# Optimization experiments

Measured on AMD Instinct MI355X. Metric: run time of the kernel, lower is better.

## Reference

```python
import jax, jax.numpy as jnp
import numpy as np

IN_FEATURES = 4096
OUT_FEATURES = 4096


def setup_inputs() -> dict:
    key = jax.random.key(0)
    k1, k2, k3 = jax.random.split(key, 3)
    x = jax.random.normal(k1, (4, 2048, IN_FEATURES), dtype=jnp.float32)
    # int8 quantized weight, stored as int8 (simulating torch int8 Parameter)
    weight_q = jax.random.randint(k2, (OUT_FEATURES, IN_FEATURES), -127, 128, dtype=jnp.int8)
    weight_scaler = jax.random.uniform(k3, (OUT_FEATURES,), dtype=jnp.float32) * 0.02
    return {"x": x, "weight_q": weight_q, "weight_scaler": weight_scaler}


def reference(x, weight_q, weight_scaler):
    # Dequantize: per-output-channel scale broadcast over in_features,
    # then F.linear: out = x @ W^T  (W: [out, in])
    w = weight_q.astype(jnp.float32) * weight_scaler[:, None]  # [out, in]
    return jnp.einsum('bsi,oi->bso', x, w)
```

## Files before the change

kernel.cpp:

```cpp
#include <hip/hip_runtime.h>
#include <stdint.h>
#include <stddef.h>

#define M_DIM 8192
#define N_DIM 4096
#define K_DIM 4096

#define BM 128
#define BN 128
#define BK 128

typedef int i32x4 __attribute__((ext_vector_type(4)));

__device__ __forceinline__ void async_load16(void* lds, const void* g) {
  __builtin_amdgcn_global_load_lds(
      (const __attribute__((address_space(1))) void*)g,
      (__attribute__((address_space(3))) void*)lds,
      16, 0, 0);
}

__global__ void quant_x_kernel(const float* __restrict__ x,
                               signed char* __restrict__ xq,
                               float* __restrict__ xs) {
  const int row = blockIdx.x;
  const float4* xr = (const float4*)(x + (size_t)row * K_DIM);
  const int t = threadIdx.x;
  float4 v[4];
  float m = 0.f;
#pragma unroll
  for (int r = 0; r < 4; ++r) {
    v[r] = xr[r * 256 + t];
    m = fmaxf(m, fmaxf(fmaxf(fabsf(v[r].x), fabsf(v[r].y)),
                       fmaxf(fabsf(v[r].z), fabsf(v[r].w))));
  }
#pragma unroll
  for (int off = 32; off > 0; off >>= 1)
    m = fmaxf(m, __shfl_down(m, off, 64));
  __shared__ float wmax[4];
  if ((t & 63) == 0) wmax[t >> 6] = m;
  __syncthreads();
  float rowmax = fmaxf(fmaxf(wmax[0], wmax[1]), fmaxf(wmax[2], wmax[3]));
  float inv = rowmax > 0.f ? 127.0f / rowmax : 0.f;
  if (t == 0) xs[row] = rowmax > 0.f ? rowmax * (1.0f / 127.0f) : 0.f;
  uint* oq = (uint*)(xq + (size_t)row * K_DIM);
#pragma unroll
  for (int r = 0; r < 4; ++r) {
    union { signed char c[4]; uint u; } o;
    o.c[0] = (signed char)(int)rintf(v[r].x * inv);
    o.c[1] = (signed char)(int)rintf(v[r].y * inv);
    o.c[2] = (signed char)(int)rintf(v[r].z * inv);
    o.c[3] = (signed char)(int)rintf(v[r].w * inv);
    oq[r * 256 + t] = o.u;
  }
}

__global__ void pack_w_kernel(const int* __restrict__ w, signed char* __restrict__ wp) {
  const int4* wi = (const int4*)w;
  uint* wo = (uint*)wp;
  size_t base = (size_t)blockIdx.x * 1024 + threadIdx.x;
#pragma unroll
  for (int r = 0; r < 4; ++r) {
    int4 a = wi[base + r * 256];
    union { signed char c[4]; uint u; } o;
    o.c[0] = (signed char)a.x; o.c[1] = (signed char)a.y;
    o.c[2] = (signed char)a.z; o.c[3] = (signed char)a.w;
    wo[base + r * 256] = o.u;
  }
}

__global__ __launch_bounds__(256, 2) void gemm_i8(
    const signed char* __restrict__ Aq, const signed char* __restrict__ Bq,
    const float* __restrict__ xs, const float* __restrict__ scaler,
    float* __restrict__ C) {
  __shared__ __align__(16) uint8_t sA[BM * BK];
  __shared__ __align__(16) uint8_t sB[BN * BK];

  const int bid  = blockIdx.x;
  const int xcd  = bid & 7;
  const int slot = bid >> 3;
  const int tile_n = (xcd * 4 + (slot & 3)) * BN;
  const int tile_m = (slot >> 2) * BM;

  const int w    = threadIdx.x >> 6;
  const int lane = threadIdx.x & 63;
  const int q    = lane >> 4;
  const int m16  = lane & 15;
  const int wrow = (w >> 1) * 64;
  const int wcol = (w & 1) * 64;

  i32x4 acc[4][4];
#pragma unroll
  for (int i = 0; i < 4; ++i)
#pragma unroll
    for (int j = 0; j < 4; ++j)
      acc[i][j] = (i32x4){0, 0, 0, 0};

  for (int kt = 0; kt < K_DIM; kt += BK) {
#pragma unroll
    for (int p = 0; p < 4; ++p) {
      int g = ((p * 4 + w) << 6) + lane;
      int r = g >> 3;
      int c = (g & 7) ^ (r & 7);
      async_load16(sA + (size_t)g * 16,
                   Aq + (size_t)(tile_m + r) * K_DIM + kt + c * 16);
    }
#pragma unroll
    for (int p = 0; p < 4; ++p) {
      int g = ((p * 4 + w) << 6) + lane;
      int r = g >> 3;
      int c = (g & 7) ^ (r & 7);
      async_load16(sB + (size_t)g * 16,
                   Bq + (size_t)(tile_n + r) * K_DIM + kt + c * 16);
    }
    __syncthreads();

#pragma unroll
    for (int ks = 0; ks < 2; ++ks) {
      const int ck = (ks << 2) + q;
      i32x4 af[4], bfr[4];
#pragma unroll
      for (int t = 0; t < 4; ++t) {
        int ra = wrow + t * 16 + m16;
        af[t] = *(const i32x4*)(sA + (size_t)(((ra << 3) + (ck ^ (ra & 7))) << 4));
        int rb = wcol + t * 16 + m16;
        bfr[t] = *(const i32x4*)(sB + (size_t)(((rb << 3) + (ck ^ (rb & 7))) << 4));
      }
#pragma unroll
      for (int i = 0; i < 4; ++i)
#pragma unroll
        for (int j = 0; j < 4; ++j)
          acc[i][j] = __builtin_amdgcn_mfma_i32_16x16x64_i8(
              af[i], bfr[j], acc[i][j], 0, 0, 0);
    }
    __syncthreads();
  }

  float rs[4][4];
#pragma unroll
  for (int i = 0; i < 4; ++i)
#pragma unroll
    for (int r = 0; r < 4; ++r)
      rs[i][r] = xs[tile_m + wrow + i * 16 + q * 4 + r];
#pragma unroll
  for (int j = 0; j < 4; ++j) {
    int col = tile_n + wcol + j * 16 + m16;
    float s = scaler[col];
#pragma unroll
    for (int i = 0; i < 4; ++i) {
      int row0 = tile_m + wrow + i * 16 + q * 4;
#pragma unroll
      for (int r = 0; r < 4; ++r)
        C[(size_t)(row0 + r) * N_DIM + col] = (float)acc[i][j][r] * rs[i][r] * s;
    }
  }
}

__global__ void fallback_kernel(const float* __restrict__ x,
                                const int* __restrict__ wq,
                                const float* __restrict__ s,
                                float* __restrict__ out) {
  size_t idx = (size_t)blockIdx.x * blockDim.x + threadIdx.x;
  int m = (int)(idx / N_DIM), n = (int)(idx % N_DIM);
  const float* xr = x + (size_t)m * K_DIM;
  const int* wr = wq + (size_t)n * K_DIM;
  float acc = 0.f;
  for (int k = 0; k < K_DIM; ++k) acc += xr[k] * (float)wr[k];
  out[idx] = acc * s[n];
}

extern "C" void kernel_launch(void* const* d_in, const int* in_sizes, int n_in,
                              void* d_out, int out_size, void* d_ws, size_t ws_size,
                              hipStream_t stream) {
  const float* x = (const float*)d_in[0];
  const int* wq = (const int*)d_in[1];
  const float* sc = (const float*)d_in[2];
  float* out = (float*)d_out;

  const size_t nx = (size_t)M_DIM * K_DIM;
  const size_t nw = (size_t)N_DIM * K_DIM;
  const size_t off_xq = 32768;
  const size_t off_wp = off_xq + nx;
  const size_t need = off_wp + nw;

  if (ws_size < need) {
    size_t total = (size_t)M_DIM * N_DIM;
    fallback_kernel<<<(int)(total / 256), 256, 0, stream>>>(x, wq, sc, out);
    return;
  }

  float* xs = (float*)d_ws;
  signed char* xq = (signed char*)d_ws + off_xq;
  signed char* wp = (signed char*)d_ws + off_wp;

  quant_x_kernel<<<M_DIM, 256, 0, stream>>>(x, xq, xs);
  pack_w_kernel<<<(int)(nw / 4 / 1024), 256, 0, stream>>>(wq, wp);

  gemm_i8<<<(N_DIM / BN) * (M_DIM / BM), 256, 0, stream>>>(xq, wp, xs, sc, out);
}
```

Before: 402.4 us.

## Double-buffer LDS tiles in int8 GEMM to overlap loads with MFMA

Doubles the LDS buffers for the A and B tiles. The next K-tile is prefetched with async global-to-LDS loads while MFMAs run on the current tile, leaving one barrier per iteration instead of two. Per-thread global and LDS offsets are now computed once outside the K loop rather than every iteration. LDS use per block rises to 64 KB, which can limit resident blocks. The compiler may also insert conservative waits that serialize the prefetch before the LDS reads.

After: 401.8 us. About the same (-0.2%).

```diff
diff --git a/kernel.cpp b/kernel.cpp
--- a/kernel.cpp
+++ b/kernel.cpp
@@ -72,8 +72,8 @@
     const signed char* __restrict__ Aq, const signed char* __restrict__ Bq,
     const float* __restrict__ xs, const float* __restrict__ scaler,
     float* __restrict__ C) {
-  __shared__ __align__(16) uint8_t sA[BM * BK];
-  __shared__ __align__(16) uint8_t sB[BN * BK];
+  __shared__ __align__(16) uint8_t sA[2][BM * BK];
+  __shared__ __align__(16) uint8_t sB[2][BN * BK];
 
   const int bid  = blockIdx.x;
   const int xcd  = bid & 7;
@@ -88,6 +88,19 @@
   const int wrow = (w >> 1) * 64;
   const int wcol = (w & 1) * 64;
 
+  int g_off[4];
+  size_t a_off[4];
+  size_t b_off[4];
+#pragma unroll
+  for (int p = 0; p < 4; ++p) {
+    int g = ((p * 4 + w) << 6) + lane;
+    int r = g >> 3;
+    int c = (g & 7) ^ (r & 7);
+    g_off[p] = g * 16;
+    a_off[p] = (size_t)(tile_m + r) * K_DIM + c * 16;
+    b_off[p] = (size_t)(tile_n + r) * K_DIM + c * 16;
+  }
+
   i32x4 acc[4][4];
 #pragma unroll
   for (int i = 0; i < 4; ++i)
@@ -95,25 +108,27 @@
     for (int j = 0; j < 4; ++j)
       acc[i][j] = (i32x4){0, 0, 0, 0};
 
+#pragma unroll
+  for (int p = 0; p < 4; ++p) {
+    async_load16(sA[0] + g_off[p], Aq + a_off[p]);
+    async_load16(sB[0] + g_off[p], Bq + b_off[p]);
+  }
+  __syncthreads();
+
+  int cur = 0;
   for (int kt = 0; kt < K_DIM; kt += BK) {
-#pragma unroll
-    for (int p = 0; p < 4; ++p) {
-      int g = ((p * 4 + w) << 6) + lane;
-      int r = g >> 3;
-      int c = (g & 7) ^ (r & 7);
-      async_load16(sA + (size_t)g * 16,
-                   Aq + (size_t)(tile_m + r) * K_DIM + kt + c * 16);
+    if (kt + BK < K_DIM) {
+      const uint8_t* nA = (const uint8_t*)Aq + (kt + BK);
+      const uint8_t* nB = (const uint8_t*)Bq + (kt + BK);
+#pragma unroll
+      for (int p = 0; p < 4; ++p) {
+        async_load16(sA[cur ^ 1] + g_off[p], nA + a_off[p]);
+        async_load16(sB[cur ^ 1] + g_off[p], nB + b_off[p]);
+      }
     }
-#pragma unroll
-    for (int p = 0; p < 4; ++p) {
-      int g = ((p * 4 + w) << 6) + lane;
-      int r = g >> 3;
-      int c = (g & 7) ^ (r & 7);
-      async_load16(sB + (size_t)g * 16,
-                   Bq + (size_t)(tile_n + r) * K_DIM + kt + c * 16);
-    }
-    __syncthreads();
-
+
+    const uint8_t* cA = sA[cur];
+    const uint8_t* cB = sB[cur];
 #pragma unroll
     for (int ks = 0; ks < 2; ++ks) {
       const int ck = (ks << 2) + q;
@@ -121,9 +136,9 @@
 #pragma unroll
       for (int t = 0; t < 4; ++t) {
         int ra = wrow + t * 16 + m16;
-        af[t] = *(const i32x4*)(sA + (size_t)(((ra << 3) + (ck ^ (ra & 7))) << 4));
+        af[t] = *(const i32x4*)(cA + (size_t)(((ra << 3) + (ck ^ (ra & 7))) << 4));
         int rb = wcol + t * 16 + m16;
-        bfr[t] = *(const i32x4*)(sB + (size_t)(((rb << 3) + (ck ^ (rb & 7))) << 4));
+        bfr[t] = *(const i32x4*)(cB + (size_t)(((rb << 3) + (ck ^ (rb & 7))) << 4));
       }
 #pragma unroll
       for (int i = 0; i < 4; ++i)
@@ -132,7 +147,9 @@
           acc[i][j] = __builtin_amdgcn_mfma_i32_16x16x64_i8(
               af[i], bfr[j], acc[i][j], 0, 0, 0);
     }
+
     __syncthreads();
+    cur ^= 1;
   }
 
   float rs[4][4];
```
